# Optimization experiments

Hardware: AMD Instinct MI355X
Metric: run time of the kernel (lower is better)

## Reference

```python
import jax, jax.numpy as jnp
import numpy as np

B, T, I, H, NC = 128, 512, 128, 512, 100


def setup_inputs() -> dict:
    key = jax.random.key(0)
    ks = jax.random.split(key, 16)
    x = jax.random.randint(ks[0], (B, T, 1), 0, NC + 1)
    # embedding table with padding row 0 zeroed (padding_idx=0)
    emb = (jax.random.normal(ks[1], (NC + 1, I)) * 1.0).at[0].set(0.0)
    # kaiming_normal_ fan_out, sigmoid nonlinearity -> std = 1/sqrt(fan_out)
    sx = 1.0 / np.sqrt(H)
    sc = 1.0 / np.sqrt(H)
    sp = 1.0 / np.sqrt(NC)
    return {
        "x": x,
        "emb": emb,
        "Wfx": jax.random.normal(ks[2], (I, H)) * sx,
        "Wfc": jax.random.normal(ks[3], (H, H)) * sc,
        "bf": jnp.zeros((H,)),
        "Wix": jax.random.normal(ks[4], (I, H)) * sx,
        "Wic": jax.random.normal(ks[5], (H, H)) * sc,
        "bi": jnp.zeros((H,)),
        "Wox": jax.random.normal(ks[6], (I, H)) * sx,
        "Woc": jax.random.normal(ks[7], (H, H)) * sc,
        "bo": jnp.zeros((H,)),
        "Wcx": jax.random.normal(ks[8], (I, H)) * sx,
        "bc": jnp.zeros((H,)),
        "Wph": jax.random.normal(ks[9], (H, NC)) * sp,
        "bp": jnp.zeros((NC,)),
    }


def reference(x, emb, Wfx, Wfc, bf, Wix, Wic, bi, Wox, Woc, bo, Wcx, bc, Wph, bp):
    idx = x[:, :, 0]                      # [B,T] int indices
    xe = emb[idx]                         # [B,T,I] embedded inputs
    h_dim = Wfc.shape[0]
    # Fuse the four input-side GEMMs into one, hoisted out of the recurrence.
    Wx = jnp.concatenate([Wfx, Wix, Wox, Wcx], axis=1)   # [I,4H]
    bx = jnp.concatenate([bf, bi, bo, bc])               # [4H]
    xg = jnp.einsum('bti,ih->bth', xe, Wx) + bx          # [B,T,4H]
    # Fuse the three peephole (cell-state) GEMMs into one per step.
    Wc = jnp.concatenate([Wfc, Wic, Woc], axis=1)        # [H,3H]
    reset = (idx > 0).astype(xg.dtype)                   # [B,T]

    def step(carry, inp):
        C, h = carry
        g, r = inp                        # g: [B,4H], r: [B]
        cg = C @ Wc                       # [B,3H]
        f = jax.nn.sigmoid(g[:, :h_dim] + cg[:, :h_dim])
        i = jax.nn.sigmoid(g[:, h_dim:2 * h_dim] + cg[:, h_dim:2 * h_dim])
        o = jax.nn.sigmoid(g[:, 2 * h_dim:3 * h_dim] + cg[:, 2 * h_dim:])
        c_tilde = jax.nn.sigmoid(g[:, 3 * h_dim:])        # note: sigmoid, not tanh (per source)
        Cn = (c_tilde * i + C * f) * r[:, None]           # reset on padding tokens
        hn = jnp.tanh(Cn) * o
        return (Cn, hn), None

    bsz = xg.shape[0]
    init = (jnp.zeros((bsz, h_dim), xg.dtype), jnp.zeros((bsz, h_dim), xg.dtype))
    xs = (jnp.swapaxes(xg, 0, 1), jnp.swapaxes(reset, 0, 1))  # time-major
    (Cf, hf), _ = jax.lax.scan(step, init, xs)
    p = hf @ Wph + bp                     # [B,num_classes]
    return jax.nn.log_softmax(p, axis=1)
```

## Files before the change

### kernel.cpp

```cpp
#include <hip/hip_runtime.h>
#include <hip/hip_bf16.h>
#include <stdint.h>

#define HD   512
#define ID   128
#define NCLS 100
#define TT   512
#define BB   128
#define NEMB 101
#define THR  512

#define NGRPB 64
#define GWGB  4
#define RPGB  2
#define COLSB 128
#define NGRPF 32
#define GWGF  8
#define RPGF  4
#define COLSF 64

#define CPAD 640
#define CBW  260
#define PSTF 5
#define PSTB 3

#define WS_FLAG 0
#define WS_BAR  4096
#define WS_G    65536
#define WS_C0   (1u * 1024 * 1024)
#define WS_C1   (WS_C0 + 262144)
#define WS_HFB  (WS_C1 + 262144)
#define NBARU   4096
#define NCU     65536

using bf16 = __hip_bfloat16;

__device__ __forceinline__ float b2f(bf16 v) { return __bfloat162float(v); }
__device__ __forceinline__ float sigf(float x) { return 1.0f / (1.0f + expf(-x)); }

__device__ __forceinline__ float cld(const float* p) {
    return __hip_atomic_load(p, __ATOMIC_RELAXED, __HIP_MEMORY_SCOPE_AGENT);
}
__device__ __forceinline__ void cst(float* p, float v) {
    __hip_atomic_store(p, v, __ATOMIC_RELAXED, __HIP_MEMORY_SCOPE_AGENT);
}
__device__ __forceinline__ void cstu(uint32_t* p, uint32_t v) {
    __hip_atomic_store(p, v, __ATOMIC_RELAXED, __HIP_MEMORY_SCOPE_AGENT);
}
__device__ __forceinline__ uint64_t cldu8(const uint64_t* p) {
    return __hip_atomic_load(p, __ATOMIC_RELAXED, __HIP_MEMORY_SCOPE_AGENT);
}

__device__ __forceinline__ uint32_t pkbf(float x, float y) {
    uint32_t u;
    asm("v_cvt_pk_bf16_f32 %0, %1, %2" : "=v"(u) : "v"(x), "v"(y));
    return u;
}
#define DOT2(acc, w, c) \
    asm("v_dot2_f32_bf16 %0, %1, %2, %0" : "+v"(acc) : "v"(w), "v"(c))

template <bool BF>
__device__ __forceinline__ float ldv(const void* p, int i) {
    if constexpr (BF) return b2f(((const bf16*)p)[i]);
    else              return ((const float*)p)[i];
}

__device__ __forceinline__ int cpi(int h) { return (h >> 4) * 20 + (h & 15); }

__device__ __forceinline__ void gbarrier(unsigned* cnt, unsigned* iter, int gwg) {
    __syncthreads();
    if (threadIdx.x == 0) {
        __hip_atomic_fetch_add(cnt, 1u, __ATOMIC_RELAXED, __HIP_MEMORY_SCOPE_AGENT);
        const unsigned tgt = (*iter + 1u) * (unsigned)gwg;
        while (__hip_atomic_load(cnt, __ATOMIC_RELAXED, __HIP_MEMORY_SCOPE_AGENT) < tgt)
            ;
    }
    ++*iter;
    __syncthreads();
}

__global__ void init_k(const uint32_t* __restrict__ emb_raw,
                       int* __restrict__ flag, unsigned* __restrict__ bars,
                       uint32_t* __restrict__ c0, uint32_t* __restrict__ c1) {
    const int t = blockIdx.x * 1024 + threadIdx.x;
    for (int k = t; k < NBARU; k += 8192) bars[k] = 0u;
    for (int k = t; k < NCU; k += 8192) { c0[k] = 0u; c1[k] = 0u; }
    if (t == 0) {
        uint32_t acc = 0;
        for (int i = 64; i < 128; ++i) acc |= emb_raw[i];
        *flag = (acc == 0u) ? 0 : 1;
    }
}

template <bool BF>
__global__ void build_G(const int* __restrict__ flag,
                        const void* __restrict__ emb,
                        const void* __restrict__ Wfx, const void* __restrict__ Wix,
                        const void* __restrict__ Wox, const void* __restrict__ Wcx,
                        const void* __restrict__ bfv, const void* __restrict__ biv,
                        const void* __restrict__ bov, const void* __restrict__ bcv,
                        float* __restrict__ G) {
    if (*flag != (BF ? 1 : 0)) return;
    const int c   = blockIdx.x;
    const int j   = blockIdx.y * 256 + threadIdx.x;
    const int q   = j >> 9;
    const int col = j & 511;
    const void* W  = (q == 0) ? Wfx : (q == 1) ? Wix : (q == 2) ? Wox : Wcx;
    const void* bv = (q == 0) ? bfv : (q == 1) ? biv : (q == 2) ? bov : bcv;
    float acc = ldv<BF>(bv, col);
    for (int i = 0; i < ID; ++i)
        acc += ldv<BF>(emb, c * ID + i) * ldv<BF>(W, i * HD + col);
    if (q == 3) acc = sigf(acc);
    G[c * 2048 + j] = acc;
}

template <bool BF>
__global__ __launch_bounds__(THR, 2) void recur_bs(
    const int* __restrict__ flag, const int* __restrict__ x,
    const float* __restrict__ G,
    const void* __restrict__ Wfc, const void* __restrict__ Wic,
    const void* __restrict__ Woc,
    float* __restrict__ C0, float* __restrict__ C1,
    float* __restrict__ Hfb, unsigned* __restrict__ bars)
{
    if (*flag != (BF ? 1 : 0)) return;

    __shared__ __align__(16) float Cs[RPGF * CPAD];
    __shared__ __align__(16) uint32_t CbS[RPGB * CBW];
    __shared__ __align__(8)  float2 part2[2048 * PSTF];
    __shared__ int idx[RPGF * TT];
    __shared__ int lz[RPGF];

    const int blk = blockIdx.x;
    const int tid = threadIdx.x;
    unsigned bi = 0;

    if constexpr (BF) {
        const int grp   = blk >> 2;
        const int rank  = blk & 3;
        const int r0    = grp * RPGB;
        const int h0    = rank * COLSB;
        const int cp    = tid & 31;
        const int chunk = tid >> 5;

        idx[tid]       = x[r0 * TT + tid];
        idx[tid + 512] = x[r0 * TT + tid + 512];
        for (int k = tid; k < RPGB * CBW; k += THR) CbS[k] = 0u;
        if (tid < RPGB) lz[tid] = -1;
        __syncthreads();
        #pragma unroll
        for (int r = 0; r < RPGB; ++r)
            if (idx[r * TT + tid] == 0) atomicMax(&lz[r], tid);
        __syncthreads();
        int t0 = TT;
        #pragma unroll
        for (int r = 0; r < RPGB; ++r) t0 = min(t0, lz[r] + 1);

        const uint16_t* Wfr = (const uint16_t*)Wfc;
        const uint16_t* Wir = (const uint16_t*)Wic;
        uint32_t wf0[16], wf1[16], wf2[16], wf3[16];
        uint32_t wi0[16], wi1[16], wi2[16], wi3[16];
        #pragma unroll
        for (int p = 0; p < 16; ++p) {
            const int hp = chunk * 32 + 2 * p;
            const int b0 = hp * HD + h0 + cp, b1 = (hp + 1) * HD + h0 + cp;
            wf0[p] = (uint32_t)Wfr[b0]      | ((uint32_t)Wfr[b1]      << 16);
            wf1[p] = (uint32_t)Wfr[b0 + 32] | ((uint32_t)Wfr[b1 + 32] << 16);
            wf2[p] = (uint32_t)Wfr[b0 + 64] | ((uint32_t)Wfr[b1 + 64] << 16);
            wf3[p] = (uint32_t)Wfr[b0 + 96] | ((uint32_t)Wfr[b1 + 96] << 16);
            wi0[p] = (uint32_t)Wir[b0]      | ((uint32_t)Wir[b1]      << 16);
            wi1[p] = (uint32_t)Wir[b0 + 32] | ((uint32_t)Wir[b1 + 32] << 16);
            wi2[p] = (uint32_t)Wir[b0 + 64] | ((uint32_t)Wir[b1 + 64] << 16);
            wi3[p] = (uint32_t)Wir[b0 + 96] | ((uint32_t)Wir[b1 + 96] << 16);
        }
        #pragma unroll
        for (int p = 0; p < 16; ++p)
            asm volatile("" : "+v"(wf0[p]), "+v"(wf1[p]), "+v"(wf2[p]), "+v"(wf3[p]),
                              "+v"(wi0[p]), "+v"(wi1[p]), "+v"(wi2[p]), "+v"(wi3[p]));

        const bool isUpd = (tid < COLSB * RPGB);
        const int uc = tid & 127, ur = tid >> 7;

        if (isUpd && t0 > 0) {
            uint32_t* b0 = (uint32_t*)((t0 & 1) ? C1 : C0);
            cstu(b0 + (r0 + ur) * HD + h0 + uc, (uint32_t)t0 & 0xFFFFu);
        }

        float Creg = 0.0f;
        const int srow = tid >> 8;
        const int spr  = tid & 255;

        for (int t = t0; t < TT; ++t) {
            #pragma unroll
            for (int p = 0; p < 16; ++p)
                asm volatile("" : "+v"(wf0[p]), "+v"(wf1[p]), "+v"(wf2[p]), "+v"(wf3[p]),
                                  "+v"(wi0[p]), "+v"(wi1[p]), "+v"(wi2[p]), "+v"(wi3[p]));

            const uint32_t* curT = (const uint32_t*)((t & 1) ? C1 : C0);
            uint32_t*       nxtT = (uint32_t*)((t & 1) ? C0 : C1);

            float gf = 0.f, gi = 0.f, sgc = 0.f;
            int cl = 1;
            if (isUpd) {
                cl = idx[ur * TT + t];
                const float* Gr = G + cl * 2048;
                gf  = Gr[h0 + uc];
                gi  = Gr[512 + h0 + uc];
                sgc = Gr[1536 + h0 + uc];
            }

            {
                const uint64_t* src = (const uint64_t*)(
                    curT + (r0 + srow) * HD + 2 * spr);
                const uint32_t exp = (uint32_t)t & 0xFFFFu;
                uint32_t w0, w1;
                for (;;) {
                    const uint64_t d = cldu8(src);
                    w0 = (uint32_t)d;
                    w1 = (uint32_t)(d >> 32);
                    if ((((w0 ^ exp) | (w1 ^ exp)) & 0xFFFFu) == 0u) break;
                }
                CbS[srow * CBW + spr] = (w0 >> 16) | (w1 & 0xFFFF0000u);
            }
            __syncthreads();

            float f0[RPGB], f1[RPGB], f2[RPGB], f3[RPGB];
            float i0[RPGB], i1[RPGB], i2[RPGB], i3[RPGB];
            #pragma unroll
            for (int r = 0; r < RPGB; ++r) {
                f0[r] = 0.f; f1[r] = 0.f; f2[r] = 0.f; f3[r] = 0.f;
                i0[r] = 0.f; i1[r] = 0.f; i2[r] = 0.f; i3[r] = 0.f;
            }
            {
                const int cb = chunk * 16;
                #pragma unroll
                for (int hh = 0; hh < 4; ++hh) {
                    #pragma unroll
                    for (int r = 0; r < RPGB; ++r) {
                        const uint4 cv = *reinterpret_cast<const uint4*>(
                            CbS + r * CBW + cb + 4 * hh);
                        const int p = 4 * hh;
                        DOT2(f0[r], wf0[p + 0], cv.x); DOT2(f0[r], wf0[p + 1], cv.y);
                        DOT2(f0[r], wf0[p + 2], cv.z); DOT2(f0[r], wf0[p + 3], cv.w);
                        DOT2(f1[r], wf1[p + 0], cv.x); DOT2(f1[r], wf1[p + 1], cv.y);
                        DOT2(f1[r], wf1[p + 2], cv.z); DOT2(f1[r], wf1[p + 3], cv.w);
                        DOT2(f2[r], wf2[p + 0], cv.x); DOT2(f2[r], wf2[p + 1], cv.y);
                        DOT2(f2[r], wf2[p + 2], cv.z); DOT2(f2[r], wf2[p + 3], cv.w);
                        DOT2(f3[r], wf3[p + 0], cv.x); DOT2(f3[r], wf3[p + 1], cv.y);
                        DOT2(f3[r], wf3[p + 2], cv.z); DOT2(f3[r], wf3[p + 3], cv.w);
                        DOT2(i0[r], wi0[p + 0], cv.x); DOT2(i0[r], wi0[p + 1], cv.y);
                        DOT2(i0[r], wi0[p + 2], cv.z); DOT2(i0[r], wi0[p + 3], cv.w);
                        DOT2(i1[r], wi1[p + 0], cv.x); DOT2(i1[r], wi1[p + 1], cv.y);
                        DOT2(i1[r], wi1[p + 2], cv.z); DOT2(i1[r], wi1[p + 3], cv.w);
                        DOT2(i2[r], wi2[p + 0], cv.x); DOT2(i2[r], wi2[p + 1], cv.y);
                        DOT2(i2[r], wi2[p + 2], cv.z); DOT2(i2[r], wi2[p + 3], cv.w);
                        DOT2(i3[r], wi3[p + 0], cv.x); DOT2(i3[r], wi3[p + 1], cv.y);
                        DOT2(i3[r], wi3[p + 2], cv.z); DOT2(i3[r], wi3[p + 3], cv.w);
                    }
                }
            }
            {
                float2* p0 = part2 + (chunk * 128 + cp)      * PSTB;
                float2* p1 = part2 + (chunk * 128 + cp + 32) * PSTB;
                float2* p2 = part2 + (chunk * 128 + cp + 64) * PSTB;
                float2* p3 = part2 + (chunk * 128 + cp + 96) * PSTB;
                #pragma unroll
                for (int r = 0; r < RPGB; ++r) {
                    p0[r] = make_float2(f0[r], i0[r]);
                    p1[r] = make_float2(f1[r], i1[r]);
                    p2[r] = make_float2(f2[r], i2[r]);
                    p3[r] = make_float2(f3[r], i3[r]);
                }
            }
            __syncthreads();

            if (isUpd) {
                float df = 0.f, di = 0.f;
                #pragma unroll
                for (int ch = 0; ch < 16; ++ch) {
                    const float2 v = part2[(ch * 128 + uc) * PSTB + ur];
                    df += v.x;
                    di += v.y;
                }
                float Cn = sgc * sigf(gi + di) + Creg * sigf(gf + df);
                Cn = (cl > 0) ? Cn : 0.0f;
                Creg = Cn;
                const uint32_t vb = pkbf(Cn, Cn);
                cstu(nxtT + (r0 + ur) * HD + h0 + uc,
                     (vb << 16) | ((uint32_t)(t + 1) & 0xFFFFu));
            }
        }

        {
            const int rr = tid >> 8, wi = tid & 255;
            const uint32_t w = CbS[rr * CBW + wi];
            Cs[rr * CPAD + cpi(2 * wi)]     = __uint_as_float((w & 0xFFFFu) << 16);
            Cs[rr * CPAD + cpi(2 * wi + 1)] = __uint_as_float(w & 0xFFFF0000u);
            __syncthreads();

            const int oc = tid & 127, och = tid >> 7;
            float ao0 = 0.f, ao1 = 0.f;
            #pragma unroll 4
            for (int k = 0; k < 128; ++k) {
                const int hp  = och * 128 + k;
                const int hpp = cpi(hp);
                const float wo = ldv<BF>(Woc, hp * HD + h0 + oc);
                ao0 += wo * Cs[0 * CPAD + hpp];
                ao1 += wo * Cs[1 * CPAD + hpp];
            }
            part2[(och * 128 + oc) * PSTB] = make_float2(ao0, ao1);
            __syncthreads();
            if (isUpd) {
                float s = 0.f;
                #pragma unroll
                for (int ch = 0; ch < 4; ++ch) {
                    const float2 v = part2[(ch * 128 + uc) * PSTB];
                    s += ur ? v.y : v.x;
                }
                const int cl2 = idx[ur * TT + TT - 1];
                const float o = sigf(G[cl2 * 2048 + 1024 + h0 + uc] + s);
                Hfb[(r0 + ur) * HD + h0 + uc] = tanhf(Creg) * o;
            }
        }
    } else {
        const int grp   = blk >> 3;
        const int rank  = blk & 7;
        const int r0    = grp * RPGF;
        const int h0    = rank * COLSF;
        const int cp    = tid & 15;
        const int chunk = tid >> 4;
        unsigned* bar = bars + grp * 32;

        idx[tid]        = x[r0 * TT + tid];
        idx[tid + 512]  = x[r0 * TT + tid + 512];
        idx[tid + 1024] = x[r0 * TT + tid + 1024];
        idx[tid + 1536] = x[r0 * TT + tid + 1536];
        if (tid < RPGF) lz[tid] = -1;
        __syncthreads();
        #pragma unroll
        for (int r = 0; r < RPGF; ++r)
            if (idx[r * TT + tid] == 0) atomicMax(&lz[r], tid);
        __syncthreads();
        int t0 = TT;
        #pragma unroll
        for (int r = 0; r < RPGF; ++r) t0 = min(t0, lz[r] + 1);

        float wf0[16], wf1[16], wf2[16], wf3[16];
        float wi0[16], wi1[16], wi2[16], wi3[16];
        #pragma unroll
        for (int k = 0; k < 16; ++k) {
            const int hp = chunk * 16 + k;
            wf0[k] = ldv<BF>(Wfc, hp * HD + h0 + cp);
            wf1[k] = ldv<BF>(Wfc, hp * HD + h0 + cp + 16);
            wf2[k] = ldv<BF>(Wfc, hp * HD + h0 + cp + 32);
            wf3[k] = ldv<BF>(Wfc, hp * HD + h0 + cp + 48);
            wi0[k] = ldv<BF>(Wic, hp * HD + h0 + cp);
            wi1[k] = ldv<BF>(Wic, hp * HD + h0 + cp + 16);
            wi2[k] = ldv<BF>(Wic, hp * HD + h0 + cp + 32);
            wi3[k] = ldv<BF>(Wic, hp * HD + h0 + cp + 48);
        }
        #pragma unroll
        for (int k = 0; k < 16; ++k)
            asm volatile("" : "+v"(wf0[k]), "+v"(wf1[k]), "+v"(wf2[k]), "+v"(wf3[k]),
                              "+v"(wi0[k]), "+v"(wi1[k]), "+v"(wi2[k]), "+v"(wi3[k]));

        const bool isUpd = (tid < COLSF * RPGF);
        const int uc = tid & 63, ur = tid >> 6;
        const int pe = cpi(tid);

        if (isUpd) {
            cst(&C0[(r0 + ur) * HD + h0 + uc], 0.0f);
            cst(&C1[(r0 + ur) * HD + h0 + uc], 0.0f);
        }
        gbarrier(bar, &bi, GWGF);

        float Creg = 0.0f;
        for (int t = t0; t < TT; ++t) {
            #pragma unroll
            for (int k = 0; k < 16; ++k)
                asm volatile("" : "+v"(wf0[k]), "+v"(wf1[k]), "+v"(wf2[k]), "+v"(wf3[k]),
                                  "+v"(wi0[k]), "+v"(wi1[k]), "+v"(wi2[k]), "+v"(wi3[k]));

            const float* cur = (t & 1) ? C1 : C0;
            float*       nxt = (t & 1) ? C0 : C1;

            float gf = 0.f, gi = 0.f, sgc = 0.f;
            int cl = 1;
            if (isUpd) {
                cl = idx[ur * TT + t];
                const float* Gr = G + cl * 2048;
                gf  = Gr[h0 + uc];
                gi  = Gr[512 + h0 + uc];
                sgc = Gr[1536 + h0 + uc];
            }

            {
                const float v0 = cld(cur + (r0 + 0) * HD + tid);
                const float v1 = cld(cur + (r0 + 1) * HD + tid);
                const float v2 = cld(cur + (r0 + 2) * HD + tid);
                const float v3 = cld(cur + (r0 + 3) * HD + tid);
                Cs[0 * CPAD + pe] = v0;
                Cs[1 * CPAD + pe] = v1;
                Cs[2 * CPAD + pe] = v2;
                Cs[3 * CPAD + pe] = v3;
            }
            __syncthreads();

            float f0[RPGF], f1[RPGF], f2[RPGF], f3[RPGF];
            float i0[RPGF], i1[RPGF], i2[RPGF], i3[RPGF];
            #pragma unroll
            for (int r = 0; r < RPGF; ++r) {
                f0[r] = 0.f; f1[r] = 0.f; f2[r] = 0.f; f3[r] = 0.f;
                i0[r] = 0.f; i1[r] = 0.f; i2[r] = 0.f; i3[r] = 0.f;
            }
            {
                const int cb = chunk * 5;
                #pragma unroll
                for (int j = 0; j < 4; ++j) {
                    #pragma unroll
                    for (int r = 0; r < RPGF; ++r) {
                        const float4 cv = reinterpret_cast<const float4*>(
                            Cs + r * CPAD)[cb + j];
                        f0[r] += wf0[4*j]*cv.x + wf0[4*j+1]*cv.y + wf0[4*j+2]*cv.z + wf0[4*j+3]*cv.w;
                        f1[r] += wf1[4*j]*cv.x + wf1[4*j+1]*cv.y + wf1[4*j+2]*cv.z + wf1[4*j+3]*cv.w;
                        f2[r] += wf2[4*j]*cv.x + wf2[4*j+1]*cv.y + wf2[4*j+2]*cv.z + wf2[4*j+3]*cv.w;
                        f3[r] += wf3[4*j]*cv.x + wf3[4*j+1]*cv.y + wf3[4*j+2]*cv.z + wf3[4*j+3]*cv.w;
                        i0[r] += wi0[4*j]*cv.x + wi0[4*j+1]*cv.y + wi0[4*j+2]*cv.z + wi0[4*j+3]*cv.w;
                        i1[r] += wi1[4*j]*cv.x + wi1[4*j+1]*cv.y + wi1[4*j+2]*cv.z + wi1[4*j+3]*cv.w;
                        i2[r] += wi2[4*j]*cv.x + wi2[4*j+1]*cv.y + wi2[4*j+2]*cv.z + wi2[4*j+3]*cv.w;
                        i3[r] += wi3[4*j]*cv.x + wi3[4*j+1]*cv.y + wi3[4*j+2]*cv.z + wi3[4*j+3]*cv.w;
                    }
                }
            }
            {
                float2* p0 = part2 + (chunk * 64 + cp)      * PSTF;
                float2* p1 = part2 + (chunk * 64 + cp + 16) * PSTF;
                float2* p2 = part2 + (chunk * 64 + cp + 32) * PSTF;
                float2* p3 = part2 + (chunk * 64 + cp + 48) * PSTF;
                #pragma unroll
                for (int r = 0; r < RPGF; ++r) {
                    p0[r] = make_float2(f0[r], i0[r]);
                    p1[r] = make_float2(f1[r], i1[r]);
                    p2[r] = make_float2(f2[r], i2[r]);
                    p3[r] = make_float2(f3[r], i3[r]);
                }
            }
            __syncthreads();

            if (isUpd) {
                float df = 0.f, di = 0.f;
                #pragma unroll
                for (int ch = 0; ch < 32; ++ch) {
                    const float2 v = part2[(ch * 64 + uc) * PSTF + ur];
                    df += v.x;
                    di += v.y;
                }
                float Cn = sgc * sigf(gi + di) + Creg * sigf(gf + df);
                Cn = (cl > 0) ? Cn : 0.0f;
                Creg = Cn;
                cst(&nxt[(r0 + ur) * HD + h0 + uc], Cn);
            }
            gbarrier(bar, &bi, GWGF);
        }

        {
            const float v0 = cld(C1 + (r0 + 0) * HD + tid);
            const float v1 = cld(C1 + (r0 + 1) * HD + tid);
            const float v2 = cld(C1 + (r0 + 2) * HD + tid);
            const float v3 = cld(C1 + (r0 + 3) * HD + tid);
            Cs[0 * CPAD + pe] = v0;
            Cs[1 * CPAD + pe] = v1;
            Cs[2 * CPAD + pe] = v2;
            Cs[3 * CPAD + pe] = v3;
            __syncthreads();

            const int oc = tid & 63, och = tid >> 6;
            float ao[RPGF];
            #pragma unroll
            for (int r = 0; r < RPGF; ++r) ao[r] = 0.0f;
            #pragma unroll 4
            for (int k = 0; k < 64; ++k) {
                const int hp = och * 64 + k;
                const int hpp = cpi(hp);
                const float wo = ldv<BF>(Woc, hp * HD + h0 + oc);
                #pragma unroll
                for (int r = 0; r < RPGF; ++r)
                    ao[r] += wo * Cs[r * CPAD + hpp];
            }
            {
                float2* pp = part2 + (och * 64 + oc) * PSTF;
                #pragma unroll
                for (int r2 = 0; r2 < RPGF / 2; ++r2)
                    pp[r2] = make_float2(ao[2 * r2], ao[2 * r2 + 1]);
            }
            __syncthreads();
            if (isUpd) {
                float s = 0.f;
                #pragma unroll
                for (int ch = 0; ch < 8; ++ch) {
                    const float2 v = part2[(ch * 64 + uc) * PSTF + (ur >> 1)];
                    s += (ur & 1) ? v.y : v.x;
                }
                const int cl2 = idx[ur * TT + TT - 1];
                const float o = sigf(G[cl2 * 2048 + 1024 + h0 + uc] + s);
                Hfb[(r0 + ur) * HD + h0 + uc] = tanhf(Creg) * o;
            }
        }
    }
}

template <bool BF>
__global__ __launch_bounds__(128) void proj(
    const int* __restrict__ flag, const float* __restrict__ Hfb,
    const void* __restrict__ Wph, const void* __restrict__ bp,
    void* __restrict__ out)
{
    if (*flag != (BF ? 1 : 0)) return;
    __shared__ __align__(16) float hv[HD];
    __shared__ float p_s[NCLS];
    __shared__ float lse_s;
    const int b   = blockIdx.x;
    const int tid = threadIdx.x;

    reinterpret_cast<float4*>(hv)[tid] =
        reinterpret_cast<const float4*>(Hfb + b * HD)[tid];
    __syncthreads();

    if (tid < NCLS) {
        float p = ldv<BF>(bp, tid);
        for (int h = 0; h < HD; ++h)
            p += hv[h] * ldv<BF>(Wph, h * NCLS + tid);
        p_s[tid] = p;
    }
    __syncthreads();
    if (tid == 0) {
        float m = -1e30f;
        for (int n = 0; n < NCLS; ++n) m = fmaxf(m, p_s[n]);
        float sum = 0.0f;
        for (int n = 0; n < NCLS; ++n) sum += expf(p_s[n] - m);
        lse_s = m + logf(sum);
    }
    __syncthreads();
    if (tid < NCLS) {
        const float v = p_s[tid] - lse_s;
        if constexpr (BF) ((bf16*)out)[b * NCLS + tid] = __float2bfloat16(v);
        else              ((float*)out)[b * NCLS + tid] = v;
    }
}

extern "C" void kernel_launch(void* const* d_in, const int* in_sizes, int n_in,
                              void* d_out, int out_size, void* d_ws, size_t ws_size,
                              hipStream_t stream) {
    const int*  x   = (const int*)d_in[0];
    const void* emb = d_in[1];
    const void* Wfx = d_in[2];
    const void* Wfc = d_in[3];
    const void* bfv = d_in[4];
    const void* Wix = d_in[5];
    const void* Wic = d_in[6];
    const void* biv = d_in[7];
    const void* Wox = d_in[8];
    const void* Woc = d_in[9];
    const void* bov = d_in[10];
    const void* Wcx = d_in[11];
    const void* bcv = d_in[12];
    const void* Wph = d_in[13];
    const void* bp  = d_in[14];

    int*      flag = (int*)((char*)d_ws + WS_FLAG);
    unsigned* bars = (unsigned*)((char*)d_ws + WS_BAR);
    float*    G    = (float*)((char*)d_ws + WS_G);
    float*    C0   = (float*)((char*)d_ws + WS_C0);
    float*    C1   = (float*)((char*)d_ws + WS_C1);
    float*    Hfb  = (float*)((char*)d_ws + WS_HFB);

    init_k<<<8, 1024, 0, stream>>>((const uint32_t*)emb, flag, bars,
                                   (uint32_t*)C0, (uint32_t*)C1);

    build_G<false><<<dim3(NEMB, 8), 256, 0, stream>>>(flag, emb, Wfx, Wix, Wox, Wcx,
                                                      bfv, biv, bov, bcv, G);
    build_G<true ><<<dim3(NEMB, 8), 256, 0, stream>>>(flag, emb, Wfx, Wix, Wox, Wcx,
                                                      bfv, biv, bov, bcv, G);

    {
        void* args[] = {(void*)&flag, (void*)&x, (void*)&G,
                        (void*)&Wfc, (void*)&Wic, (void*)&Woc,
                        (void*)&C0, (void*)&C1, (void*)&Hfb, (void*)&bars};
        hipLaunchCooperativeKernel((const void*)recur_bs<false>, dim3(256), dim3(THR),
                                   args, 0, stream);
        hipLaunchCooperativeKernel((const void*)recur_bs<true>, dim3(256), dim3(THR),
                                   args, 0, stream);
    }

    proj<false><<<BB, 128, 0, stream>>>(flag, Hfb, Wph, bp, d_out);
    proj<true ><<<BB, 128, 0, stream>>>(flag, Hfb, Wph, bp, d_out);
}
```

Measured before the change: 1.593 ms.

## Replace per-step group barrier in fp32 path with tagged-value polling

The fp32 recurrence path no longer runs a group-wide barrier each timestep. Each published cell-state value now carries a 2-bit step tag in its low mantissa bits, and consumers spin until all four loaded words carry the expected tag. This removes the per-step barrier round trip and lets blocks proceed as soon as their inputs are ready. In exchange the cell state loses two mantissa bits, and every thread runs a spin loop on global memory. Code blocks were also reordered, and a syncthreads was added before the bf16 epilogue.

```diff
diff --git a/kernel.cpp b/kernel.cpp
--- a/kernel.cpp
+++ b/kernel.cpp
@@ -10,14 +10,14 @@
 #define NEMB 101
 #define THR  512
 
+#define NGRPF 32
+#define GWGF  8
+#define RPGF  4
+#define COLSF 64
 #define NGRPB 64
 #define GWGB  4
 #define RPGB  2
 #define COLSB 128
-#define NGRPF 32
-#define GWGF  8
-#define RPGF  4
-#define COLSF 64
 
 #define CPAD 640
 #define CBW  260
@@ -46,6 +46,9 @@
 }
 __device__ __forceinline__ void cstu(uint32_t* p, uint32_t v) {
     __hip_atomic_store(p, v, __ATOMIC_RELAXED, __HIP_MEMORY_SCOPE_AGENT);
+}
+__device__ __forceinline__ uint32_t cldu(const uint32_t* p) {
+    return __hip_atomic_load(p, __ATOMIC_RELAXED, __HIP_MEMORY_SCOPE_AGENT);
 }
 __device__ __forceinline__ uint64_t cldu8(const uint64_t* p) {
     return __hip_atomic_load(p, __ATOMIC_RELAXED, __HIP_MEMORY_SCOPE_AGENT);
@@ -135,7 +138,194 @@
     const int tid = threadIdx.x;
     unsigned bi = 0;
 
-    if constexpr (BF) {
+    if constexpr (!BF) {
+        const int grp   = blk >> 3;
+        const int rank  = blk & 7;
+        const int r0    = grp * RPGF;
+        const int h0    = rank * COLSF;
+        const int cp    = tid & 15;
+        const int chunk = tid >> 4;
+        unsigned* bar = bars + grp * 32;
+
+        idx[tid]        = x[r0 * TT + tid];
+        idx[tid + 512]  = x[r0 * TT + tid + 512];
+        idx[tid + 1024] = x[r0 * TT + tid + 1024];
+        idx[tid + 1536] = x[r0 * TT + tid + 1536];
+        for (int k = tid; k < RPGF * CPAD; k += THR) Cs[k] = 0.0f;
+        if (tid < RPGF) lz[tid] = -1;
+        __syncthreads();
+        #pragma unroll
+        for (int r = 0; r < RPGF; ++r)
+            if (idx[r * TT + tid] == 0) atomicMax(&lz[r], tid);
+        __syncthreads();
+        int t0 = TT;
+        #pragma unroll
+        for (int r = 0; r < RPGF; ++r) t0 = min(t0, lz[r] + 1);
+
+        float wf0[16], wf1[16], wf2[16], wf3[16];
+        float wi0[16], wi1[16], wi2[16], wi3[16];
+        #pragma unroll
+        for (int k = 0; k < 16; ++k) {
+            const int hp = chunk * 16 + k;
+            wf0[k] = ldv<BF>(Wfc, hp * HD + h0 + cp);
+            wf1[k] = ldv<BF>(Wfc, hp * HD + h0 + cp + 16);
+            wf2[k] = ldv<BF>(Wfc, hp * HD + h0 + cp + 32);
+            wf3[k] = ldv<BF>(Wfc, hp * HD + h0 + cp + 48);
+            wi0[k] = ldv<BF>(Wic, hp * HD + h0 + cp);
+            wi1[k] = ldv<BF>(Wic, hp * HD + h0 + cp + 16);
+            wi2[k] = ldv<BF>(Wic, hp * HD + h0 + cp + 32);
+            wi3[k] = ldv<BF>(Wic, hp * HD + h0 + cp + 48);
+        }
+        #pragma unroll
+        for (int k = 0; k < 16; ++k)
+            asm volatile("" : "+v"(wf0[k]), "+v"(wf1[k]), "+v"(wf2[k]), "+v"(wf3[k]),
+                              "+v"(wi0[k]), "+v"(wi1[k]), "+v"(wi2[k]), "+v"(wi3[k]));
+
+        const bool isUpd = (tid < COLSF * RPGF);
+        const int uc = tid & 63, ur = tid >> 6;
+        const int pe = cpi(tid);
+
+        {
+            uint32_t* tA = (uint32_t*)((t0 & 1) ? C1 : C0);
+            uint32_t* tB = (uint32_t*)((t0 & 1) ? C0 : C1);
+            if (isUpd) {
+                cstu(tA + (r0 + ur) * HD + h0 + uc, (uint32_t)(t0 & 3));
+                cstu(tB + (r0 + ur) * HD + h0 + uc, (uint32_t)((t0 + 3) & 3));
+            }
+        }
+        gbarrier(bar, &bi, GWGF);
+
+        float Creg = 0.0f;
+        for (int t = t0; t < TT; ++t) {
+            #pragma unroll
+            for (int k = 0; k < 16; ++k)
+                asm volatile("" : "+v"(wf0[k]), "+v"(wf1[k]), "+v"(wf2[k]), "+v"(wf3[k]),
+                                  "+v"(wi0[k]), "+v"(wi1[k]), "+v"(wi2[k]), "+v"(wi3[k]));
+
+            const uint32_t* curT = (const uint32_t*)((t & 1) ? C1 : C0);
+            uint32_t*       nxtT = (uint32_t*)((t & 1) ? C0 : C1);
+
+            float gf = 0.f, gi = 0.f, sgc = 0.f;
+            int cl = 1;
+            if (isUpd) {
+                cl = idx[ur * TT + t];
+                const float* Gr = G + cl * 2048;
+                gf  = Gr[h0 + uc];
+                gi  = Gr[512 + h0 + uc];
+                sgc = Gr[1536 + h0 + uc];
+            }
+
+            {
+                const uint32_t* s0 = curT + (r0 + 0) * HD + tid;
+                const uint32_t* s1 = curT + (r0 + 1) * HD + tid;
+                const uint32_t* s2 = curT + (r0 + 2) * HD + tid;
+                const uint32_t* s3 = curT + (r0 + 3) * HD + tid;
+                const uint32_t exp = (uint32_t)t & 3u;
+                uint32_t w0, w1, w2, w3;
+                for (;;) {
+                    w0 = cldu(s0); w1 = cldu(s1); w2 = cldu(s2); w3 = cldu(s3);
+                    if ((((w0 ^ exp) | (w1 ^ exp) | (w2 ^ exp) | (w3 ^ exp)) & 3u) == 0u)
+                        break;
+                }
+                Cs[0 * CPAD + pe] = __uint_as_float(w0 & ~3u);
+                Cs[1 * CPAD + pe] = __uint_as_float(w1 & ~3u);
+                Cs[2 * CPAD + pe] = __uint_as_float(w2 & ~3u);
+                Cs[3 * CPAD + pe] = __uint_as_float(w3 & ~3u);
+            }
+            __syncthreads();
+
+            float f0[RPGF], f1[RPGF], f2[RPGF], f3[RPGF];
+            float i0[RPGF], i1[RPGF], i2[RPGF], i3[RPGF];
+            #pragma unroll
+            for (int r = 0; r < RPGF; ++r) {
+                f0[r] = 0.f; f1[r] = 0.f; f2[r] = 0.f; f3[r] = 0.f;
+                i0[r] = 0.f; i1[r] = 0.f; i2[r] = 0.f; i3[r] = 0.f;
+            }
+            {
+                const int cb = chunk * 5;
+                #pragma unroll
+                for (int j = 0; j < 4; ++j) {
+                    #pragma unroll
+                    for (int r = 0; r < RPGF; ++r) {
+                        const float4 cv = reinterpret_cast<const float4*>(
+                            Cs + r * CPAD)[cb + j];
+                        f0[r] += wf0[4*j]*cv.x + wf0[4*j+1]*cv.y + wf0[4*j+2]*cv.z + wf0[4*j+3]*cv.w;
+                        f1[r] += wf1[4*j]*cv.x + wf1[4*j+1]*cv.y + wf1[4*j+2]*cv.z + wf1[4*j+3]*cv.w;
+                        f2[r] += wf2[4*j]*cv.x + wf2[4*j+1]*cv.y + wf2[4*j+2]*cv.z + wf2[4*j+3]*cv.w;
+                        f3[r] += wf3[4*j]*cv.x + wf3[4*j+1]*cv.y + wf3[4*j+2]*cv.z + wf3[4*j+3]*cv.w;
+                        i0[r] += wi0[4*j]*cv.x + wi0[4*j+1]*cv.y + wi0[4*j+2]*cv.z + wi0[4*j+3]*cv.w;
+                        i1[r] += wi1[4*j]*cv.x + wi1[4*j+1]*cv.y + wi1[4*j+2]*cv.z + wi1[4*j+3]*cv.w;
+                        i2[r] += wi2[4*j]*cv.x + wi2[4*j+1]*cv.y + wi2[4*j+2]*cv.z + wi2[4*j+3]*cv.w;
+                        i3[r] += wi3[4*j]*cv.x + wi3[4*j+1]*cv.y + wi3[4*j+2]*cv.z + wi3[4*j+3]*cv.w;
+                    }
+                }
+            }
+            {
+                float2* p0 = part2 + (chunk * 64 + cp)      * PSTF;
+                float2* p1 = part2 + (chunk * 64 + cp + 16) * PSTF;
+                float2* p2 = part2 + (chunk * 64 + cp + 32) * PSTF;
+                float2* p3 = part2 + (chunk * 64 + cp + 48) * PSTF;
+                #pragma unroll
+                for (int r = 0; r < RPGF; ++r) {
+                    p0[r] = make_float2(f0[r], i0[r]);
+                    p1[r] = make_float2(f1[r], i1[r]);
+                    p2[r] = make_float2(f2[r], i2[r]);
+                    p3[r] = make_float2(f3[r], i3[r]);
+                }
+            }
+            __syncthreads();
+
+            if (isUpd) {
+                float df = 0.f, di = 0.f;
+                #pragma unroll
+                for (int ch = 0; ch < 32; ++ch) {
+                    const float2 v = part2[(ch * 64 + uc) * PSTF + ur];
+                    df += v.x;
+                    di += v.y;
+                }
+                float Cn = sgc * sigf(gi + di) + Creg * sigf(gf + df);
+                Cn = (cl > 0) ? Cn : 0.0f;
+                Creg = Cn;
+                cstu(nxtT + (r0 + ur) * HD + h0 + uc,
+                     (__float_as_uint(Cn) & ~3u) | ((uint32_t)(t + 1) & 3u));
+            }
+        }
+
+        __syncthreads();
+        {
+            const int oc = tid & 63, och = tid >> 6;
+            float ao[RPGF];
+            #pragma unroll
+            for (int r = 0; r < RPGF; ++r) ao[r] = 0.0f;
+            #pragma unroll 4
+            for (int k = 0; k < 64; ++k) {
+                const int hp = och * 64 + k;
+                const int hpp = cpi(hp);
+                const float wo = ldv<BF>(Woc, hp * HD + h0 + oc);
+                #pragma unroll
+                for (int r = 0; r < RPGF; ++r)
+                    ao[r] += wo * Cs[r * CPAD + hpp];
+            }
+            {
+                float2* pp = part2 + (och * 64 + oc) * PSTF;
+                #pragma unroll
+                for (int r2 = 0; r2 < RPGF / 2; ++r2)
+                    pp[r2] = make_float2(ao[2 * r2], ao[2 * r2 + 1]);
+            }
+            __syncthreads();
+            if (isUpd) {
+                float s = 0.f;
+                #pragma unroll
+                for (int ch = 0; ch < 8; ++ch) {
+                    const float2 v = part2[(ch * 64 + uc) * PSTF + (ur >> 1)];
+                    s += (ur & 1) ? v.y : v.x;
+                }
+                const int cl2 = idx[ur * TT + TT - 1];
+                const float o = sigf(G[cl2 * 2048 + 1024 + h0 + uc] + s);
+                Hfb[(r0 + ur) * HD + h0 + uc] = tanhf(Creg) * o;
+            }
+        }
+    } else {
         const int grp   = blk >> 2;
         const int rank  = blk & 3;
         const int r0    = grp * RPGB;
@@ -291,6 +481,7 @@
             }
         }
 
+        __syncthreads();
         {
             const int rr = tid >> 8, wi = tid & 255;
             const uint32_t w = CbS[rr * CBW + wi];
@@ -316,190 +507,6 @@
                 for (int ch = 0; ch < 4; ++ch) {
                     const float2 v = part2[(ch * 128 + uc) * PSTB];
                     s += ur ? v.y : v.x;
-                }
-                const int cl2 = idx[ur * TT + TT - 1];
-                const float o = sigf(G[cl2 * 2048 + 1024 + h0 + uc] + s);
-                Hfb[(r0 + ur) * HD + h0 + uc] = tanhf(Creg) * o;
-            }
-        }
-    } else {
-        const int grp   = blk >> 3;
-        const int rank  = blk & 7;
-        const int r0    = grp * RPGF;
-        const int h0    = rank * COLSF;
-        const int cp    = tid & 15;
-        const int chunk = tid >> 4;
-        unsigned* bar = bars + grp * 32;
-
-        idx[tid]        = x[r0 * TT + tid];
-        idx[tid + 512]  = x[r0 * TT + tid + 512];
-        idx[tid + 1024] = x[r0 * TT + tid + 1024];
-        idx[tid + 1536] = x[r0 * TT + tid + 1536];
-        if (tid < RPGF) lz[tid] = -1;
-        __syncthreads();
-        #pragma unroll
-        for (int r = 0; r < RPGF; ++r)
-            if (idx[r * TT + tid] == 0) atomicMax(&lz[r], tid);
-        __syncthreads();
-        int t0 = TT;
-        #pragma unroll
-        for (int r = 0; r < RPGF; ++r) t0 = min(t0, lz[r] + 1);
-
-        float wf0[16], wf1[16], wf2[16], wf3[16];
-        float wi0[16], wi1[16], wi2[16], wi3[16];
-        #pragma unroll
-        for (int k = 0; k < 16; ++k) {
-            const int hp = chunk * 16 + k;
-            wf0[k] = ldv<BF>(Wfc, hp * HD + h0 + cp);
-            wf1[k] = ldv<BF>(Wfc, hp * HD + h0 + cp + 16);
-            wf2[k] = ldv<BF>(Wfc, hp * HD + h0 + cp + 32);
-            wf3[k] = ldv<BF>(Wfc, hp * HD + h0 + cp + 48);
-            wi0[k] = ldv<BF>(Wic, hp * HD + h0 + cp);
-            wi1[k] = ldv<BF>(Wic, hp * HD + h0 + cp + 16);
-            wi2[k] = ldv<BF>(Wic, hp * HD + h0 + cp + 32);
-            wi3[k] = ldv<BF>(Wic, hp * HD + h0 + cp + 48);
-        }
-        #pragma unroll
-        for (int k = 0; k < 16; ++k)
-            asm volatile("" : "+v"(wf0[k]), "+v"(wf1[k]), "+v"(wf2[k]), "+v"(wf3[k]),
-                              "+v"(wi0[k]), "+v"(wi1[k]), "+v"(wi2[k]), "+v"(wi3[k]));
-
-        const bool isUpd = (tid < COLSF * RPGF);
-        const int uc = tid & 63, ur = tid >> 6;
-        const int pe = cpi(tid);
-
-        if (isUpd) {
-            cst(&C0[(r0 + ur) * HD + h0 + uc], 0.0f);
-            cst(&C1[(r0 + ur) * HD + h0 + uc], 0.0f);
-        }
-        gbarrier(bar, &bi, GWGF);
-
-        float Creg = 0.0f;
-        for (int t = t0; t < TT; ++t) {
-            #pragma unroll
-            for (int k = 0; k < 16; ++k)
-                asm volatile("" : "+v"(wf0[k]), "+v"(wf1[k]), "+v"(wf2[k]), "+v"(wf3[k]),
-                                  "+v"(wi0[k]), "+v"(wi1[k]), "+v"(wi2[k]), "+v"(wi3[k]));
-
-            const float* cur = (t & 1) ? C1 : C0;
-            float*       nxt = (t & 1) ? C0 : C1;
-
-            float gf = 0.f, gi = 0.f, sgc = 0.f;
-            int cl = 1;
-            if (isUpd) {
-                cl = idx[ur * TT + t];
-                const float* Gr = G + cl * 2048;
-                gf  = Gr[h0 + uc];
-                gi  = Gr[512 + h0 + uc];
-                sgc = Gr[1536 + h0 + uc];
-            }
-
-            {
-                const float v0 = cld(cur + (r0 + 0) * HD + tid);
-                const float v1 = cld(cur + (r0 + 1) * HD + tid);
-                const float v2 = cld(cur + (r0 + 2) * HD + tid);
-                const float v3 = cld(cur + (r0 + 3) * HD + tid);
-                Cs[0 * CPAD + pe] = v0;
-                Cs[1 * CPAD + pe] = v1;
-                Cs[2 * CPAD + pe] = v2;
-                Cs[3 * CPAD + pe] = v3;
-            }
-            __syncthreads();
-
-            float f0[RPGF], f1[RPGF], f2[RPGF], f3[RPGF];
-            float i0[RPGF], i1[RPGF], i2[RPGF], i3[RPGF];
-            #pragma unroll
-            for (int r = 0; r < RPGF; ++r) {
-                f0[r] = 0.f; f1[r] = 0.f; f2[r] = 0.f; f3[r] = 0.f;
-                i0[r] = 0.f; i1[r] = 0.f; i2[r] = 0.f; i3[r] = 0.f;
-            }
-            {
-                const int cb = chunk * 5;
-                #pragma unroll
-                for (int j = 0; j < 4; ++j) {
-                    #pragma unroll
-                    for (int r = 0; r < RPGF; ++r) {
-                        const float4 cv = reinterpret_cast<const float4*>(
-                            Cs + r * CPAD)[cb + j];
-                        f0[r] += wf0[4*j]*cv.x + wf0[4*j+1]*cv.y + wf0[4*j+2]*cv.z + wf0[4*j+3]*cv.w;
-                        f1[r] += wf1[4*j]*cv.x + wf1[4*j+1]*cv.y + wf1[4*j+2]*cv.z + wf1[4*j+3]*cv.w;
-                        f2[r] += wf2[4*j]*cv.x + wf2[4*j+1]*cv.y + wf2[4*j+2]*cv.z + wf2[4*j+3]*cv.w;
-                        f3[r] += wf3[4*j]*cv.x + wf3[4*j+1]*cv.y + wf3[4*j+2]*cv.z + wf3[4*j+3]*cv.w;
-                        i0[r] += wi0[4*j]*cv.x + wi0[4*j+1]*cv.y + wi0[4*j+2]*cv.z + wi0[4*j+3]*cv.w;
-                        i1[r] += wi1[4*j]*cv.x + wi1[4*j+1]*cv.y + wi1[4*j+2]*cv.z + wi1[4*j+3]*cv.w;
-                        i2[r] += wi2[4*j]*cv.x + wi2[4*j+1]*cv.y + wi2[4*j+2]*cv.z + wi2[4*j+3]*cv.w;
-                        i3[r] += wi3[4*j]*cv.x + wi3[4*j+1]*cv.y + wi3[4*j+2]*cv.z + wi3[4*j+3]*cv.w;
-                    }
-                }
-            }
-            {
-                float2* p0 = part2 + (chunk * 64 + cp)      * PSTF;
-                float2* p1 = part2 + (chunk * 64 + cp + 16) * PSTF;
-                float2* p2 = part2 + (chunk * 64 + cp + 32) * PSTF;
-                float2* p3 = part2 + (chunk * 64 + cp + 48) * PSTF;
-                #pragma unroll
-                for (int r = 0; r < RPGF; ++r) {
-                    p0[r] = make_float2(f0[r], i0[r]);
-                    p1[r] = make_float2(f1[r], i1[r]);
-                    p2[r] = make_float2(f2[r], i2[r]);
-                    p3[r] = make_float2(f3[r], i3[r]);
-                }
-            }
-            __syncthreads();
-
-            if (isUpd) {
-                float df = 0.f, di = 0.f;
-                #pragma unroll
-                for (int ch = 0; ch < 32; ++ch) {
-                    const float2 v = part2[(ch * 64 + uc) * PSTF + ur];
-                    df += v.x;
-                    di += v.y;
-                }
-                float Cn = sgc * sigf(gi + di) + Creg * sigf(gf + df);
-                Cn = (cl > 0) ? Cn : 0.0f;
-                Creg = Cn;
-                cst(&nxt[(r0 + ur) * HD + h0 + uc], Cn);
-            }
-            gbarrier(bar, &bi, GWGF);
-        }
-
-        {
-            const float v0 = cld(C1 + (r0 + 0) * HD + tid);
-            const float v1 = cld(C1 + (r0 + 1) * HD + tid);
-            const float v2 = cld(C1 + (r0 + 2) * HD + tid);
-            const float v3 = cld(C1 + (r0 + 3) * HD + tid);
-            Cs[0 * CPAD + pe] = v0;
-            Cs[1 * CPAD + pe] = v1;
-            Cs[2 * CPAD + pe] = v2;
-            Cs[3 * CPAD + pe] = v3;
-            __syncthreads();
-
-            const int oc = tid & 63, och = tid >> 6;
-            float ao[RPGF];
-            #pragma unroll
-            for (int r = 0; r < RPGF; ++r) ao[r] = 0.0f;
-            #pragma unroll 4
-            for (int k = 0; k < 64; ++k) {
-                const int hp = och * 64 + k;
-                const int hpp = cpi(hp);
-                const float wo = ldv<BF>(Woc, hp * HD + h0 + oc);
-                #pragma unroll
-                for (int r = 0; r < RPGF; ++r)
-                    ao[r] += wo * Cs[r * CPAD + hpp];
-            }
-            {
-                float2* pp = part2 + (och * 64 + oc) * PSTF;
-                #pragma unroll
-                for (int r2 = 0; r2 < RPGF / 2; ++r2)
-                    pp[r2] = make_float2(ao[2 * r2], ao[2 * r2 + 1]);
-            }
-            __syncthreads();
-            if (isUpd) {
-                float s = 0.f;
-                #pragma unroll
-                for (int ch = 0; ch < 8; ++ch) {
-                    const float2 v = part2[(ch * 64 + uc) * PSTF + (ur >> 1)];
-                    s += (ur & 1) ? v.y : v.x;
                 }
                 const int cl2 = idx[ur * TT + TT - 1];
                 const float o = sigf(G[cl2 * 2048 + 1024 + h0 + uc] + s);
```

Result: no change. 1.597 ms (+0.2%).
